# Optimization experiments

Measured on AMD Instinct MI355X. Metric: run time of the kernel, lower is better.

Reference implementation:

```python
import jax, jax.numpy as jnp
import numpy as np
from jax import lax

PATCH = 9
DILATION = 1
EPS = 1e-6


def _l2norm(x):
    # L2-normalize over channel dim (dim=1), eps added to sum of squares before sqrt
    norm = jnp.sqrt(jnp.sum(x * x, axis=1, keepdims=True) + EPS)
    return x / norm


def setup_inputs() -> dict:
    key = jax.random.key(0)
    k1, k2 = jax.random.split(key)
    feature1 = jax.random.normal(k1, (4, 64, 64, 64), dtype=jnp.float32)
    feature2 = jax.random.normal(k2, (4, 64, 64, 64), dtype=jnp.float32)
    return {"feature1": feature1, "feature2": feature2}


def _correlation(f1, f2, patch, dilation):
    # SpatialCorrelationSampler with ks=1, stride=1, pad=0:
    # corr[b, pi, pj, y, x] = sum_c f1[b,c,y,x] * f2[b,c,y+dy,x+dx]
    # dy = (pi - patch//2)*dilation, dx = (pj - patch//2)*dilation; OOB = 0.
    b, c, h, w = f1.shape
    half = (patch // 2) * dilation
    f2p = jnp.pad(f2, ((0, 0), (0, 0), (half, half), (half, half)))
    d = jnp.arange(patch, dtype=jnp.int32) * dilation  # offsets into padded map
    offs = jnp.stack(jnp.meshgrid(d, d, indexing="ij"), axis=-1).reshape(-1, 2)  # [P^2, 2]

    def one_disp(off):
        f2s = lax.dynamic_slice(f2p, (0, 0, off[0], off[1]), (b, c, h, w))
        return jnp.sum(f1 * f2s, axis=1)  # [b, h, w]

    corr = lax.map(one_disp, offs)  # [P^2, b, h, w] (sequential -> low peak memory)
    return jnp.transpose(corr, (1, 0, 2, 3))  # [b, P^2, h, w]


def reference(feature1, feature2):
    f1 = _l2norm(feature1)
    f2 = _l2norm(feature2)
    b, c, h, w = f1.shape
    corr = _correlation(f1, f2, PATCH, DILATION)  # [b, P^2, h, w]
    corr = corr.reshape(b, PATCH * PATCH, h * w)
    return jax.nn.relu(corr)
```

## Files before the change

### kernel.cpp

```cpp
#include <hip/hip_runtime.h>

#define BB 4
#define CC 64
#define C2 32
#define HH 64
#define WW 64
#define PATCH 9
#define HALF 4
#define P2 81
#define HW 4096
#define IMG (CC * HW)

typedef _Float16 v2h __attribute__((ext_vector_type(2)));

static __device__ __forceinline__ unsigned pk(float a, float b) {
    v2h h = {(_Float16)a, (_Float16)b};
    return __builtin_bit_cast(unsigned, h);
}

__global__ __launch_bounds__(576) void corr_kernel(const float* __restrict__ f1,
                                                   const float* __restrict__ f2,
                                                   float* __restrict__ out) {
    __shared__ unsigned sB[PATCH * C2 * 72];
    __shared__ unsigned sA[C2 * 64];
    __shared__ float sS2[PATCH * 72];
    __shared__ float sS1[64];

    const int tid = threadIdx.x;
    const int x  = tid & 63;
    const int dy = tid >> 6;
    const int b  = blockIdx.x >> 6;
    const int y  = blockIdx.x & 63;

    const float* f1r = f1 + b * IMG + y * WW;
    const float* f2b = f2 + b * IMG;

    if (tid < 512) {
        int c2 = tid >> 4, k = tid & 15;
        float4 va = *(const float4*)(f1r + (2 * c2) * HW + 4 * k);
        float4 vb = *(const float4*)(f1r + (2 * c2 + 1) * HW + 4 * k);
        uint4 u = {pk(va.x, vb.x), pk(va.y, vb.y), pk(va.z, vb.z), pk(va.w, vb.w)};
        *(uint4*)&sA[c2 * 64 + 4 * k] = u;
    }
#pragma unroll
    for (int it = 0; it < 8; ++it) {
        int item = tid + it * 576;
        int dyy = item >> 9;
        int rem = item & 511;
        int c2 = rem >> 4, k = rem & 15;
        int y2 = y + dyy - HALF;
        uint4 u = {0u, 0u, 0u, 0u};
        if ((unsigned)y2 < HH) {
            const float* p = f2b + y2 * WW + 4 * k;
            float4 va = *(const float4*)(p + (2 * c2) * HW);
            float4 vb = *(const float4*)(p + (2 * c2 + 1) * HW);
            u.x = pk(va.x, vb.x); u.y = pk(va.y, vb.y);
            u.z = pk(va.z, vb.z); u.w = pk(va.w, vb.w);
        }
        *(uint4*)&sB[(dyy * C2 + c2) * 72 + 4 + 4 * k] = u;
    }
#pragma unroll
    for (int j = tid; j < 2304; j += 576) {
        int row = j >> 3, e = j & 7;
        sB[row * 72 + (e < 4 ? e : 64 + e)] = 0u;
    }
    __syncthreads();

    for (int t = tid; t < 712; t += 576) {
        float ss = 0.f;
        if (t < 648) {
            int row = t / 72, col = t - row * 72;
            const unsigned* p = &sB[row * C2 * 72 + col];
#pragma unroll
            for (int c2 = 0; c2 < C2; ++c2) {
                v2h v = __builtin_bit_cast(v2h, p[c2 * 72]);
                ss = __builtin_amdgcn_fdot2(v, v, ss, false);
            }
            sS2[t] = rsqrtf(ss + 1e-6f);
        } else {
            int col = t - 648;
            const unsigned* p = &sA[col];
#pragma unroll
            for (int c2 = 0; c2 < C2; ++c2) {
                v2h v = __builtin_bit_cast(v2h, p[c2 * 64]);
                ss = __builtin_amdgcn_fdot2(v, v, ss, false);
            }
            sS1[col] = rsqrtf(ss + 1e-6f);
        }
    }
    __syncthreads();

    float acc[PATCH];
#pragma unroll
    for (int i = 0; i < PATCH; ++i) acc[i] = 0.f;
#pragma unroll
    for (int c2 = 0; c2 < C2; ++c2) {
        v2h a2 = __builtin_bit_cast(v2h, sA[c2 * 64 + x]);
        const unsigned* br = &sB[(dy * C2 + c2) * 72 + x];
#pragma unroll
        for (int dx = 0; dx < PATCH; ++dx)
            acc[dx] = __builtin_amdgcn_fdot2(a2, __builtin_bit_cast(v2h, br[dx]),
                                             acc[dx], false);
    }

    const float s1 = sS1[x];
    float* ob = out + b * P2 * HW + y * WW + x;
#pragma unroll
    for (int dx = 0; dx < PATCH; ++dx)
        ob[(dy * PATCH + dx) * HW] = fmaxf(acc[dx] * s1 * sS2[dy * 72 + x + dx], 0.f);
}

extern "C" void kernel_launch(void* const* d_in, const int* in_sizes, int n_in,
                              void* d_out, int out_size, void* d_ws, size_t ws_size,
                              hipStream_t stream) {
    const float* f1 = (const float*)d_in[0];
    const float* f2 = (const float*)d_in[1];
    float* out = (float*)d_out;
    (void)d_ws; (void)ws_size;

    corr_kernel<<<BB * HH, 576, 0, stream>>>(f1, f2, out);
}
```

Before: 70.34 us.

## Split correlation work into one 64-thread block per (b, y, dy) row

The kernel now launches 2304 single-wavefront blocks instead of 256 blocks of 576 threads, each handling one displacement row dy. Each thread keeps its f1 column in registers and computes its f1 norm there. The f2 norm comes from the center tap of the shared tile, and blocks whose shifted row is out of bounds just write zeros. This is meant to raise occupancy and drop the separate norm pass and the large shared buffer, at the cost of f1 being reloaded nine times and more blocks to launch.

```diff
diff --git a/kernel.cpp b/kernel.cpp
--- a/kernel.cpp
+++ b/kernel.cpp
@@ -18,96 +18,83 @@
     return __builtin_bit_cast(unsigned, h);
 }
 
-__global__ __launch_bounds__(576) void corr_kernel(const float* __restrict__ f1,
-                                                   const float* __restrict__ f2,
-                                                   float* __restrict__ out) {
-    __shared__ unsigned sB[PATCH * C2 * 72];
-    __shared__ unsigned sA[C2 * 64];
-    __shared__ float sS2[PATCH * 72];
-    __shared__ float sS1[64];
+__global__ __launch_bounds__(64) void corr_kernel(const float* __restrict__ f1,
+                                                  const float* __restrict__ f2,
+                                                  float* __restrict__ out) {
+    __shared__ unsigned sB[C2 * 72];
+    __shared__ float sS2[64];
 
-    const int tid = threadIdx.x;
-    const int x  = tid & 63;
-    const int dy = tid >> 6;
-    const int b  = blockIdx.x >> 6;
-    const int y  = blockIdx.x & 63;
+    const int x   = threadIdx.x;
+    const int bid = blockIdx.x;
+    const int dy  = bid % PATCH;
+    const int y   = (bid / PATCH) & 63;
+    const int b   = bid / (PATCH * HH);
+    const int y2  = y + dy - HALF;
 
-    const float* f1r = f1 + b * IMG + y * WW;
-    const float* f2b = f2 + b * IMG;
+    float* ob = out + b * (P2 * HW) + y * WW + x;
 
-    if (tid < 512) {
-        int c2 = tid >> 4, k = tid & 15;
-        float4 va = *(const float4*)(f1r + (2 * c2) * HW + 4 * k);
-        float4 vb = *(const float4*)(f1r + (2 * c2 + 1) * HW + 4 * k);
+    if ((unsigned)y2 >= HH) {
+#pragma unroll
+        for (int dx = 0; dx < PATCH; ++dx)
+            ob[(dy * PATCH + dx) * HW] = 0.f;
+        return;
+    }
+
+    const float* f1r = f1 + b * IMG + y * WW + x;
+    unsigned a[C2];
+    float ssq1 = 0.f;
+#pragma unroll
+    for (int c2 = 0; c2 < C2; ++c2) {
+        float u0 = f1r[(2 * c2) * HW];
+        float u1 = f1r[(2 * c2 + 1) * HW];
+        ssq1 = fmaf(u0, u0, fmaf(u1, u1, ssq1));
+        a[c2] = pk(u0, u1);
+    }
+
+    const float* f2r = f2 + b * IMG + y2 * WW;
+#pragma unroll
+    for (int it = 0; it < 8; ++it) {
+        int item = x + it * 64;
+        int c2 = item >> 4, k = item & 15;
+        const float* p = f2r + 4 * k;
+        float4 va = *(const float4*)(p + (2 * c2) * HW);
+        float4 vb = *(const float4*)(p + (2 * c2 + 1) * HW);
         uint4 u = {pk(va.x, vb.x), pk(va.y, vb.y), pk(va.z, vb.z), pk(va.w, vb.w)};
-        *(uint4*)&sA[c2 * 64 + 4 * k] = u;
+        *(uint4*)&sB[c2 * 72 + 4 + 4 * k] = u;
     }
 #pragma unroll
-    for (int it = 0; it < 8; ++it) {
-        int item = tid + it * 576;
-        int dyy = item >> 9;
-        int rem = item & 511;
-        int c2 = rem >> 4, k = rem & 15;
-        int y2 = y + dyy - HALF;
-        uint4 u = {0u, 0u, 0u, 0u};
-        if ((unsigned)y2 < HH) {
-            const float* p = f2b + y2 * WW + 4 * k;
-            float4 va = *(const float4*)(p + (2 * c2) * HW);
-            float4 vb = *(const float4*)(p + (2 * c2 + 1) * HW);
-            u.x = pk(va.x, vb.x); u.y = pk(va.y, vb.y);
-            u.z = pk(va.z, vb.z); u.w = pk(va.w, vb.w);
-        }
-        *(uint4*)&sB[(dyy * C2 + c2) * 72 + 4 + 4 * k] = u;
-    }
-#pragma unroll
-    for (int j = tid; j < 2304; j += 576) {
-        int row = j >> 3, e = j & 7;
-        sB[row * 72 + (e < 4 ? e : 64 + e)] = 0u;
-    }
-    __syncthreads();
-
-    for (int t = tid; t < 712; t += 576) {
-        float ss = 0.f;
-        if (t < 648) {
-            int row = t / 72, col = t - row * 72;
-            const unsigned* p = &sB[row * C2 * 72 + col];
-#pragma unroll
-            for (int c2 = 0; c2 < C2; ++c2) {
-                v2h v = __builtin_bit_cast(v2h, p[c2 * 72]);
-                ss = __builtin_amdgcn_fdot2(v, v, ss, false);
-            }
-            sS2[t] = rsqrtf(ss + 1e-6f);
-        } else {
-            int col = t - 648;
-            const unsigned* p = &sA[col];
-#pragma unroll
-            for (int c2 = 0; c2 < C2; ++c2) {
-                v2h v = __builtin_bit_cast(v2h, p[c2 * 64]);
-                ss = __builtin_amdgcn_fdot2(v, v, ss, false);
-            }
-            sS1[col] = rsqrtf(ss + 1e-6f);
-        }
+    for (int it = 0; it < 4; ++it) {
+        int j = x + it * 64;
+        int c2 = j >> 3, e = j & 7;
+        sB[c2 * 72 + (e < 4 ? e : 64 + e)] = 0u;
     }
     __syncthreads();
 
     float acc[PATCH];
 #pragma unroll
     for (int i = 0; i < PATCH; ++i) acc[i] = 0.f;
+    float ssq2 = 0.f;
 #pragma unroll
     for (int c2 = 0; c2 < C2; ++c2) {
-        v2h a2 = __builtin_bit_cast(v2h, sA[c2 * 64 + x]);
-        const unsigned* br = &sB[(dy * C2 + c2) * 72 + x];
+        v2h a2 = __builtin_bit_cast(v2h, a[c2]);
+        const unsigned* br = &sB[c2 * 72 + x];
 #pragma unroll
         for (int dx = 0; dx < PATCH; ++dx)
             acc[dx] = __builtin_amdgcn_fdot2(a2, __builtin_bit_cast(v2h, br[dx]),
                                              acc[dx], false);
+        v2h c4 = __builtin_bit_cast(v2h, br[4]);
+        ssq2 = __builtin_amdgcn_fdot2(c4, c4, ssq2, false);
     }
+    sS2[x] = rsqrtf(ssq2 + 1e-6f);
+    __syncthreads();
 
-    const float s1 = sS1[x];
-    float* ob = out + b * P2 * HW + y * WW + x;
+    const float s1 = rsqrtf(ssq1 + 1e-6f);
 #pragma unroll
-    for (int dx = 0; dx < PATCH; ++dx)
-        ob[(dy * PATCH + dx) * HW] = fmaxf(acc[dx] * s1 * sS2[dy * 72 + x + dx], 0.f);
+    for (int dx = 0; dx < PATCH; ++dx) {
+        int col = x + dx - HALF;
+        col = min(max(col, 0), WW - 1);
+        ob[(dy * PATCH + dx) * HW] = fmaxf(acc[dx] * s1 * sS2[col], 0.f);
+    }
 }
 
 extern "C" void kernel_launch(void* const* d_in, const int* in_sizes, int n_in,
@@ -118,5 +105,5 @@
     float* out = (float*)d_out;
     (void)d_ws; (void)ws_size;
 
-    corr_kernel<<<BB * HH, 576, 0, stream>>>(f1, f2, out);
+    corr_kernel<<<BB * HH * PATCH, 64, 0, stream>>>(f1, f2, out);
 }
```

After: 67.88 us. 3.5% less time.
